# Kernel optimization log

Measured on AMD Instinct MI355X. Metric: run time of the kernel, lower is better.

The kernel has to match this reference:

```python
import jax, jax.numpy as jnp
import numpy as np

# Fixed DAG: chain 0 -> 1 -> ... -> 7 -> leaf. One activation per node.
NUM_NODES = 8          # intermediate nodes (node 7's only child is the leaf)
NUM_EDGES = NUM_NODES - 1
ACTS = ['tanh', 'relu', 'tanh', 'sigmoid', 'identity', 'relu', 'tanh', 'identity']
MAX_NORM = 25.0

_ACT_FNS = {
    'relu': jax.nn.relu,
    'tanh': jnp.tanh,
    'sigmoid': jax.nn.sigmoid,
    'identity': lambda x: x,
}


def setup_inputs() -> dict:
    key = jax.random.key(0)
    ks = jax.random.split(key, 10)
    T, B, ninp, nhid = 128, 512, 256, 256
    r = 0.1  # init_weights(0.1) uniform range
    u = lambda k, shape: jax.random.uniform(k, shape, jnp.float32, -r, r)
    return {
        'inputs': jax.random.normal(ks[0], (T, B, ninp), jnp.float32),
        'hidden': jax.random.normal(ks[1], (B, nhid), jnp.float32),
        'w_xc_w': u(ks[2], (nhid, ninp)),
        'w_xc_b': u(ks[3], (nhid,)),
        'w_xh_w': u(ks[4], (nhid, ninp)),
        'w_xh_b': u(ks[5], (nhid,)),
        'w_hc': u(ks[6], (nhid, nhid)),
        'w_hh': u(ks[7], (nhid, nhid)),
        'Wc': u(ks[8], (NUM_EDGES, nhid, nhid)),  # per-edge c-gate weights (no bias)
        'Wh': u(ks[9], (NUM_EDGES, nhid, nhid)),  # per-edge h weights (no bias)
    }


def _cell(x_t, h_prev, w_xc_w, w_xc_b, w_xh_w, w_xh_b, w_hc, w_hh, Wc, Wh):
    # node 0 (torch Linear convention: x @ W.T + b)
    c0 = jax.nn.sigmoid(x_t @ w_xc_w.T + w_xc_b + h_prev @ w_hc.T)
    f0 = _ACT_FNS[ACTS[0]]
    h = c0 * f0(x_t @ w_xh_w.T + w_xh_b + h_prev @ w_hh.T) + (1.0 - c0) * h_prev
    # chain of nodes 1..NUM_NODES-1 (fixed, small loop -> unrolled under jit)
    for e in range(NUM_EDGES):
        c = jax.nn.sigmoid(h @ Wc[e].T)
        f = _ACT_FNS[ACTS[e + 1]]
        h = c * f(h @ Wh[e].T) + (1.0 - c) * h
    # single leaf node -> mean over leaves is identity
    return h


def reference(inputs, hidden, w_xc_w, w_xc_b, w_xh_w, w_xh_b, w_hc, w_hh, Wc, Wh):
    def step(h_prev, x_t):
        out = _cell(x_t, h_prev, w_xc_w, w_xc_b, w_xh_w, w_xh_b, w_hc, w_hh, Wc, Wh)
        # NORM hidden-mode clipping: rescale rows with norm > MAX_NORM (mask is
        # computed from .data in torch, i.e. no gradient through the scale)
        norms = jnp.linalg.norm(out, axis=-1)
        scale = jax.lax.stop_gradient(jnp.where(norms > MAX_NORM, MAX_NORM / norms, 1.0))
        out = out * scale[:, None]
        return out, out  # (new hidden, per-step output) -- output == hidden here

    hidden_final, outs = jax.lax.scan(step, hidden, inputs)
    T, B, nhid = outs.shape
    outputs = outs.reshape(T * B, nhid)  # torch.cat along dim 0
    return outputs, hidden_final
```

## Files before the change

kernel.cpp:

```cpp
#include <hip/hip_runtime.h>
#include <stdint.h>


#define T_STEPS 128
#define B_ROWS  512
#define NH      256
#define NPAIRS  9
#define KQ      64

__device__ __forceinline__ float sigmoidf_(float x){
  float e = __expf(-fabsf(x));
  float s = 1.f/(1.f+e);
  return x>=0.f ? s : 1.f-s;
}
__device__ __forceinline__ float tanhf_(float x){
  float e = __expf(-2.f*fabsf(x));
  float r = (1.f-e)/(1.f+e);
  return x>=0.f ? r : -r;
}
__device__ __forceinline__ unsigned short f2bf(float f){
  uint32_t u = __float_as_uint(f);
  uint32_t r = (u + 0x7fffu + ((u>>16)&1u)) >> 16;
  return (unsigned short)r;
}
__device__ __forceinline__ uint32_t packbf(float a, float b){
  return (uint32_t)f2bf(a) | ((uint32_t)f2bf(b) << 16);
}
__device__ __forceinline__ float bfhi(float f){
  return __uint_as_float((uint32_t)f2bf(f) << 16);
}
__device__ __forceinline__ float dot2bf(uint32_t a, uint32_t b, float c){
  float d;
  asm("v_dot2_f32_bf16 %0, %1, %2, %3" : "=v"(d) : "v"(a), "v"(b), "v"(c));
  return d;
}

__global__ void prep_weights(const float* __restrict__ wxc, const float* __restrict__ wxh,
                             const float* __restrict__ whc, const float* __restrict__ whh,
                             const float* __restrict__ Wc,  const float* __restrict__ Wh,
                             uint32_t* __restrict__ WQ){
  int idx = blockIdx.x*256 + threadIdx.x;
  if (idx >= NPAIRS*KQ*NH*4) return;
  int p   = idx >> 16;
  int rem = idx & 65535;
  int kq  = rem >> 10;
  int n   = (rem >> 2) & 255;
  int c   = rem & 3;
  int mat = c & 1;
  int k0  = 4*kq + 2*(c>>1);
  const float *A, *B;
  if (p == 0)      { A = wxc; B = wxh; }
  else if (p == 1) { A = whc; B = whh; }
  else             { A = Wc + (size_t)(p-2)*NH*NH; B = Wh + (size_t)(p-2)*NH*NH; }
  const float* M = mat ? B : A;
  WQ[idx] = packbf(M[(size_t)n*NH + k0], M[(size_t)n*NH + k0 + 1]);
}

__device__ __forceinline__ void stream_q(const uint4* __restrict__ wj,
                                         const uint4* __restrict__ src,
                                         float& accA, float& accB){
  float a0=0.f,b0=0.f,a1=0.f,b1=0.f,a2=0.f,b2=0.f,a3=0.f,b3=0.f;
  #pragma unroll 8
  for (int kq = 0; kq < KQ; ++kq){
    uint4 w  = wj[(size_t)kq*NH];
    uint4 hv = src[kq];
    a0 = dot2bf(w.x, hv.x, a0);  b0 = dot2bf(w.y, hv.x, b0);
    a1 = dot2bf(w.z, hv.y, a1);  b1 = dot2bf(w.w, hv.y, b1);
    a2 = dot2bf(w.x, hv.z, a2);  b2 = dot2bf(w.y, hv.z, b2);
    a3 = dot2bf(w.z, hv.w, a3);  b3 = dot2bf(w.w, hv.w, b3);
  }
  accA += (a0 + a1) + (a2 + a3);
  accB += (b0 + b1) + (b2 + b3);
}

template<int ACT>
__device__ __forceinline__ float edge_hn(const uint4* __restrict__ wj,
                                         const uint4* __restrict__ src, float hold){
  float accA = 0.f, accB = 0.f;
  stream_q(wj, src, accA, accB);
  float c = sigmoidf_(accA);
  float f;
  if constexpr (ACT==0)      f = fmaxf(accB, 0.f);
  else if constexpr (ACT==1) f = tanhf_(accB);
  else if constexpr (ACT==2) f = sigmoidf_(accB);
  else                       f = accB;
  return c*f + (1.f-c)*hold;
}

__global__ __launch_bounds__(512) void dag_main(
    const float* __restrict__ x,
    const float* __restrict__ h0,
    const float* __restrict__ bxc,
    const float* __restrict__ bxh,
    const uint32_t* __restrict__ WQ,
    float* __restrict__ out)
{
  __shared__ float hf[2][NH];
  __shared__ uint4 hq[2][KQ];
  __shared__ uint4 xq[2][KQ];
  __shared__ float red[8];

  const int tid = threadIdx.x;
  const int j   = tid & 255;
  const int r   = tid >> 8;
  const int wv  = tid >> 6;
  const int r0  = blockIdx.x * 2;
  const uint4* WQ4 = (const uint4*)WQ;

  const int prr = tid >> 8;
  const int pc  = tid & 3;
  const int pk0 = ((tid >> 2) & 63)*4 + 2*(pc & 1);

  const float bc = bxc[j], bh = bxh[j];

  hf[r][j] = h0[(size_t)(r0 + r)*NH + j];
  __syncthreads();
  {
    float2 hp = *(const float2*)&hf[prr][pk0];
    uint32_t d = (pc < 2) ? packbf(hp.x, hp.y)
                          : packbf(hp.x - bfhi(hp.x), hp.y - bfhi(hp.y));
    ((uint32_t*)hq)[tid] = d;
    const float2 xv = *(const float2*)&x[(size_t)(r0 + prr)*NH + pk0];
    uint32_t dx = (pc < 2) ? packbf(xv.x, xv.y)
                           : packbf(xv.x - bfhi(xv.x), xv.y - bfhi(xv.y));
    ((uint32_t*)xq)[tid] = dx;
  }
  __syncthreads();

  for (int t = 0; t < T_STEPS; ++t){
    {
      float accA = 0.f, accB = 0.f;
      stream_q(WQ4 + (size_t)0*KQ*NH + j, xq[r], accA, accB);
      stream_q(WQ4 + (size_t)1*KQ*NH + j, hq[r], accA, accB);
      float hold = hf[r][j];
      float c0 = sigmoidf_(accA + bc);
      float f0 = tanhf_(accB + bh);
      hf[r][j] = c0*f0 + (1.f-c0)*hold;
    }
    __syncthreads();
    {
      float2 hp = *(const float2*)&hf[prr][pk0];
      ((uint32_t*)hq)[tid] = (pc < 2) ? packbf(hp.x, hp.y)
                                      : packbf(hp.x - bfhi(hp.x), hp.y - bfhi(hp.y));
    }
    __syncthreads();

    #define EDGE_STAGE(P, ACT)                                                   \
    hf[r][j] = edge_hn<ACT>(WQ4 + (size_t)(P)*KQ*NH + j, hq[r], hf[r][j]);       \
    __syncthreads();                                                             \
    {                                                                            \
      float2 hp = *(const float2*)&hf[prr][pk0];                                 \
      ((uint32_t*)hq)[tid] = (pc < 2) ? packbf(hp.x, hp.y)                       \
                                      : packbf(hp.x - bfhi(hp.x), hp.y - bfhi(hp.y)); \
    }                                                                            \
    __syncthreads();

    EDGE_STAGE(2, 0)
    EDGE_STAGE(3, 1)
    EDGE_STAGE(4, 2)
    EDGE_STAGE(5, 3)
    EDGE_STAGE(6, 0)
    EDGE_STAGE(7, 1)
    #undef EDGE_STAGE

    {
      float hn = edge_hn<3>(WQ4 + (size_t)8*KQ*NH + j, hq[r], hf[r][j]);
      float pw = hn*hn;
      #pragma unroll
      for (int off = 32; off; off >>= 1) pw += __shfl_xor(pw, off);
      if ((tid & 63) == 0) red[wv] = pw;
      __syncthreads();
      float s2  = red[r*4] + red[r*4+1] + red[r*4+2] + red[r*4+3];
      float nrm = sqrtf(s2);
      float sc  = (nrm > 25.f) ? 25.f/nrm : 1.f;
      float hv  = hn * sc;
      out[(size_t)t*(B_ROWS*NH) + (size_t)(r0+r)*NH + j] = hv;
      hf[r][j] = hv;
    }
    __syncthreads();
    {
      float2 hp = *(const float2*)&hf[prr][pk0];
      ((uint32_t*)hq)[tid] = (pc < 2) ? packbf(hp.x, hp.y)
                                      : packbf(hp.x - bfhi(hp.x), hp.y - bfhi(hp.y));
      if (t + 1 < T_STEPS){
        const float2 xv = *(const float2*)&x[((size_t)(t+1)*B_ROWS + r0 + prr)*NH + pk0];
        ((uint32_t*)xq)[tid] = (pc < 2) ? packbf(xv.x, xv.y)
                                        : packbf(xv.x - bfhi(xv.x), xv.y - bfhi(xv.y));
      }
    }
    __syncthreads();
  }

  out[(size_t)T_STEPS*(B_ROWS*NH) + (size_t)(r0+r)*NH + j] = hf[r][j];
}

extern "C" void kernel_launch(void* const* d_in, const int* in_sizes, int n_in,
                              void* d_out, int out_size, void* d_ws, size_t ws_size,
                              hipStream_t stream) {
  const float* x   = (const float*)d_in[0];
  const float* h0  = (const float*)d_in[1];
  const float* wxc = (const float*)d_in[2];
  const float* bxc = (const float*)d_in[3];
  const float* wxh = (const float*)d_in[4];
  const float* bxh = (const float*)d_in[5];
  const float* whc = (const float*)d_in[6];
  const float* whh = (const float*)d_in[7];
  const float* Wc  = (const float*)d_in[8];
  const float* Wh  = (const float*)d_in[9];
  uint32_t* WQ = (uint32_t*)d_ws;

  const int total = NPAIRS*KQ*NH*4;
  prep_weights<<<(total + 255)/256, 256, 0, stream>>>(wxc, wxh, whc, whh, Wc, Wh, WQ);
  dag_main<<<B_ROWS/2, 512, 0, stream>>>(x, h0, bxc, bxh, WQ, (float*)d_out);
}
```

Measured before the change: 4.788 ms.

## Switch to fp16 dot2, process four rows per block with split-K across waves

Replaces the bf16 hi/lo split representation with a single fp16 pack and v_dot2_f32_f16, halving the dot products per weight. Each 1024-thread block now handles four batch rows, with the K dimension split into four slices whose partial sums are reduced through shared memory, so every weight load is reused across four rows. Packing of h now uses wave shuffles instead of shared-memory reads. This costs some precision from fp16 rounding and adds a reduction step per stage, plus only a quarter of threads run the activations.

```diff
diff --git a/kernel.cpp b/kernel.cpp
--- a/kernel.cpp
+++ b/kernel.cpp
@@ -1,4 +1,5 @@
 #include <hip/hip_runtime.h>
+#include <hip/hip_fp16.h>
 #include <stdint.h>
 
 
@@ -7,6 +8,11 @@
 #define NH      256
 #define NPAIRS  9
 #define KQ      64
+#define BM      4
+#define NBLK    (B_ROWS/BM)
+#define NTHR    1024
+#define SQ      4
+#define QPS     (KQ/SQ)
 
 __device__ __forceinline__ float sigmoidf_(float x){
   float e = __expf(-fabsf(x));
@@ -18,20 +24,15 @@
   float r = (1.f-e)/(1.f+e);
   return x>=0.f ? r : -r;
 }
-__device__ __forceinline__ unsigned short f2bf(float f){
-  uint32_t u = __float_as_uint(f);
-  uint32_t r = (u + 0x7fffu + ((u>>16)&1u)) >> 16;
-  return (unsigned short)r;
-}
-__device__ __forceinline__ uint32_t packbf(float a, float b){
-  return (uint32_t)f2bf(a) | ((uint32_t)f2bf(b) << 16);
-}
-__device__ __forceinline__ float bfhi(float f){
-  return __uint_as_float((uint32_t)f2bf(f) << 16);
-}
-__device__ __forceinline__ float dot2bf(uint32_t a, uint32_t b, float c){
+__device__ __forceinline__ unsigned short f2h(float f){
+  return __half_as_ushort(__float2half(f));
+}
+__device__ __forceinline__ uint32_t packh(float a, float b){
+  return (uint32_t)f2h(a) | ((uint32_t)f2h(b) << 16);
+}
+__device__ __forceinline__ float fdot2_(uint32_t a, uint32_t b, float c){
   float d;
-  asm("v_dot2_f32_bf16 %0, %1, %2, %3" : "=v"(d) : "v"(a), "v"(b), "v"(c));
+  asm("v_dot2_f32_f16 %0, %1, %2, %3" : "=v"(d) : "v"(a), "v"(b), "v"(c));
   return d;
 }
 
@@ -53,41 +54,59 @@
   else if (p == 1) { A = whc; B = whh; }
   else             { A = Wc + (size_t)(p-2)*NH*NH; B = Wh + (size_t)(p-2)*NH*NH; }
   const float* M = mat ? B : A;
-  WQ[idx] = packbf(M[(size_t)n*NH + k0], M[(size_t)n*NH + k0 + 1]);
-}
-
-__device__ __forceinline__ void stream_q(const uint4* __restrict__ wj,
-                                         const uint4* __restrict__ src,
-                                         float& accA, float& accB){
-  float a0=0.f,b0=0.f,a1=0.f,b1=0.f,a2=0.f,b2=0.f,a3=0.f,b3=0.f;
-  #pragma unroll 8
-  for (int kq = 0; kq < KQ; ++kq){
-    uint4 w  = wj[(size_t)kq*NH];
-    uint4 hv = src[kq];
-    a0 = dot2bf(w.x, hv.x, a0);  b0 = dot2bf(w.y, hv.x, b0);
-    a1 = dot2bf(w.z, hv.y, a1);  b1 = dot2bf(w.w, hv.y, b1);
-    a2 = dot2bf(w.x, hv.z, a2);  b2 = dot2bf(w.y, hv.z, b2);
-    a3 = dot2bf(w.z, hv.w, a3);  b3 = dot2bf(w.w, hv.w, b3);
-  }
-  accA += (a0 + a1) + (a2 + a3);
-  accB += (b0 + b1) + (b2 + b3);
+  WQ[idx] = packh(M[(size_t)n*NH + k0], M[(size_t)n*NH + k0 + 1]);
 }
 
 template<int ACT>
-__device__ __forceinline__ float edge_hn(const uint4* __restrict__ wj,
-                                         const uint4* __restrict__ src, float hold){
-  float accA = 0.f, accB = 0.f;
-  stream_q(wj, src, accA, accB);
-  float c = sigmoidf_(accA);
-  float f;
-  if constexpr (ACT==0)      f = fmaxf(accB, 0.f);
-  else if constexpr (ACT==1) f = tanhf_(accB);
-  else if constexpr (ACT==2) f = sigmoidf_(accB);
-  else                       f = accB;
-  return c*f + (1.f-c)*hold;
-}
-
-__global__ __launch_bounds__(512) void dag_main(
+__device__ __forceinline__ float actf(float v){
+  if constexpr (ACT==0)      return fmaxf(v, 0.f);
+  else if constexpr (ACT==1) return tanhf_(v);
+  else if constexpr (ACT==2) return sigmoidf_(v);
+  else                       return v;
+}
+
+__device__ __forceinline__ void stream16(const uint4* __restrict__ wp,
+                                         const uint4 (* __restrict__ src)[2],
+                                         int qb, float* acc){
+  #pragma unroll 4
+  for (int q = 0; q < QPS; ++q){
+    const uint4 w  = wp[(size_t)q*NH];
+    const uint4 ha = src[qb+q][0];
+    const uint4 hb = src[qb+q][1];
+    acc[0]  = fdot2_(w.x, ha.x, acc[0]);
+    acc[1]  = fdot2_(w.z, ha.y, acc[1]);
+    acc[2]  = fdot2_(w.y, ha.x, acc[2]);
+    acc[3]  = fdot2_(w.w, ha.y, acc[3]);
+    acc[4]  = fdot2_(w.x, ha.z, acc[4]);
+    acc[5]  = fdot2_(w.z, ha.w, acc[5]);
+    acc[6]  = fdot2_(w.y, ha.z, acc[6]);
+    acc[7]  = fdot2_(w.w, ha.w, acc[7]);
+    acc[8]  = fdot2_(w.x, hb.x, acc[8]);
+    acc[9]  = fdot2_(w.z, hb.y, acc[9]);
+    acc[10] = fdot2_(w.y, hb.x, acc[10]);
+    acc[11] = fdot2_(w.w, hb.y, acc[11]);
+    acc[12] = fdot2_(w.x, hb.z, acc[12]);
+    acc[13] = fdot2_(w.z, hb.w, acc[13]);
+    acc[14] = fdot2_(w.y, hb.z, acc[14]);
+    acc[15] = fdot2_(w.w, hb.w, acc[15]);
+  }
+}
+
+__device__ __forceinline__ void pack_hq(uint4 (*hq)[2], int j, const float* hn){
+  uint4 v0, v1;
+  float b1, b2, b3;
+  b1=__shfl_down(hn[0],1); b2=__shfl_down(hn[0],2); b3=__shfl_down(hn[0],3);
+  v0.x = packh(hn[0], b1); v0.y = packh(b2, b3);
+  b1=__shfl_down(hn[1],1); b2=__shfl_down(hn[1],2); b3=__shfl_down(hn[1],3);
+  v0.z = packh(hn[1], b1); v0.w = packh(b2, b3);
+  b1=__shfl_down(hn[2],1); b2=__shfl_down(hn[2],2); b3=__shfl_down(hn[2],3);
+  v1.x = packh(hn[2], b1); v1.y = packh(b2, b3);
+  b1=__shfl_down(hn[3],1); b2=__shfl_down(hn[3],2); b3=__shfl_down(hn[3],3);
+  v1.z = packh(hn[3], b1); v1.w = packh(b2, b3);
+  if ((j & 3) == 0){ hq[j>>2][0] = v0; hq[j>>2][1] = v1; }
+}
+
+__global__ __launch_bounds__(NTHR) void dag_main(
     const float* __restrict__ x,
     const float* __restrict__ h0,
     const float* __restrict__ bxc,
@@ -95,65 +114,94 @@
     const uint32_t* __restrict__ WQ,
     float* __restrict__ out)
 {
-  __shared__ float hf[2][NH];
-  __shared__ uint4 hq[2][KQ];
-  __shared__ uint4 xq[2][KQ];
-  __shared__ float red[8];
+  __shared__ uint4  hq[KQ][2];
+  __shared__ uint4  xq[KQ][2];
+  __shared__ float4 part[SQ][NH][2];
+  __shared__ float  red[4][BM];
 
   const int tid = threadIdx.x;
   const int j   = tid & 255;
-  const int r   = tid >> 8;
-  const int wv  = tid >> 6;
-  const int r0  = blockIdx.x * 2;
-  const uint4* WQ4 = (const uint4*)WQ;
-
-  const int prr = tid >> 8;
-  const int pc  = tid & 3;
-  const int pk0 = ((tid >> 2) & 63)*4 + 2*(pc & 1);
-
-  const float bc = bxc[j], bh = bxh[j];
-
-  hf[r][j] = h0[(size_t)(r0 + r)*NH + j];
+  const int s   = tid >> 8;
+  const int qb  = s * QPS;
+  const int r0  = blockIdx.x * BM;
+  const uint4* WQ4   = (const uint4*)WQ;
+  const uint4* wbase = WQ4 + (size_t)qb*NH + j;
+
+  float hold[BM] = {0.f,0.f,0.f,0.f};
+  float bc = 0.f, bh = 0.f;
+  if (tid < 256){
+    bc = bxc[j]; bh = bxh[j];
+    #pragma unroll
+    for (int r = 0; r < BM; ++r) hold[r] = h0[(size_t)(r0+r)*NH + j];
+    pack_hq(hq, j, hold);
+  }
+  if (s == 3){
+    #pragma unroll
+    for (int i = 0; i < 2; ++i){
+      int d  = j + i*256;
+      int rr = d >> 7, kp = d & 127;
+      const float2 xv = *(const float2*)&x[(size_t)(r0+rr)*NH + 2*kp];
+      int kq = kp>>1, hh = rr>>1, comp = ((rr&1)<<1) | (kp&1);
+      ((uint32_t*)xq)[kq*8 + hh*4 + comp] = packh(xv.x, xv.y);
+    }
+  }
   __syncthreads();
-  {
-    float2 hp = *(const float2*)&hf[prr][pk0];
-    uint32_t d = (pc < 2) ? packbf(hp.x, hp.y)
-                          : packbf(hp.x - bfhi(hp.x), hp.y - bfhi(hp.y));
-    ((uint32_t*)hq)[tid] = d;
-    const float2 xv = *(const float2*)&x[(size_t)(r0 + prr)*NH + pk0];
-    uint32_t dx = (pc < 2) ? packbf(xv.x, xv.y)
-                           : packbf(xv.x - bfhi(xv.x), xv.y - bfhi(xv.y));
-    ((uint32_t*)xq)[tid] = dx;
-  }
-  __syncthreads();
+
+  #define STORE_PART(acc) \
+    part[s][j][0] = make_float4(acc[0]+acc[1],  acc[4]+acc[5],  acc[8]+acc[9],   acc[12]+acc[13]); \
+    part[s][j][1] = make_float4(acc[2]+acc[3],  acc[6]+acc[7],  acc[10]+acc[11], acc[14]+acc[15]);
+
+  #define SUM_PART(Av, Bv) \
+    float Av[4] = {0,0,0,0}, Bv[4] = {0,0,0,0}; \
+    _Pragma("unroll") \
+    for (int ss = 0; ss < SQ; ++ss){ \
+      float4 pa = part[ss][j][0], pb = part[ss][j][1]; \
+      Av[0]+=pa.x; Av[1]+=pa.y; Av[2]+=pa.z; Av[3]+=pa.w; \
+      Bv[0]+=pb.x; Bv[1]+=pb.y; Bv[2]+=pb.z; Bv[3]+=pb.w; \
+    }
 
   for (int t = 0; t < T_STEPS; ++t){
     {
-      float accA = 0.f, accB = 0.f;
-      stream_q(WQ4 + (size_t)0*KQ*NH + j, xq[r], accA, accB);
-      stream_q(WQ4 + (size_t)1*KQ*NH + j, hq[r], accA, accB);
-      float hold = hf[r][j];
-      float c0 = sigmoidf_(accA + bc);
-      float f0 = tanhf_(accB + bh);
-      hf[r][j] = c0*f0 + (1.f-c0)*hold;
-    }
-    __syncthreads();
-    {
-      float2 hp = *(const float2*)&hf[prr][pk0];
-      ((uint32_t*)hq)[tid] = (pc < 2) ? packbf(hp.x, hp.y)
-                                      : packbf(hp.x - bfhi(hp.x), hp.y - bfhi(hp.y));
-    }
-    __syncthreads();
-
-    #define EDGE_STAGE(P, ACT)                                                   \
-    hf[r][j] = edge_hn<ACT>(WQ4 + (size_t)(P)*KQ*NH + j, hq[r], hf[r][j]);       \
-    __syncthreads();                                                             \
-    {                                                                            \
-      float2 hp = *(const float2*)&hf[prr][pk0];                                 \
-      ((uint32_t*)hq)[tid] = (pc < 2) ? packbf(hp.x, hp.y)                       \
-                                      : packbf(hp.x - bfhi(hp.x), hp.y - bfhi(hp.y)); \
-    }                                                                            \
-    __syncthreads();
+      float acc[16] = {};
+      stream16(wbase,                    xq, qb, acc);
+      stream16(wbase + (size_t)1*KQ*NH,  hq, qb, acc);
+      STORE_PART(acc)
+      __syncthreads();
+      if (tid < 256){
+        SUM_PART(Av, Bv)
+        float hn[BM];
+        #pragma unroll
+        for (int r = 0; r < BM; ++r){
+          float c = sigmoidf_(Av[r] + bc);
+          float f = tanhf_(Bv[r] + bh);
+          hn[r] = c*f + (1.f-c)*hold[r];
+          hold[r] = hn[r];
+        }
+        pack_hq(hq, j, hn);
+      }
+      __syncthreads();
+    }
+
+    #define EDGE_STAGE(P, ACT_)                                   \
+    {                                                             \
+      float acc[16] = {};                                         \
+      stream16(wbase + (size_t)(P)*KQ*NH, hq, qb, acc);           \
+      STORE_PART(acc)                                             \
+      __syncthreads();                                            \
+      if (tid < 256){                                             \
+        SUM_PART(Av, Bv)                                          \
+        float hn[BM];                                             \
+        _Pragma("unroll")                                         \
+        for (int r = 0; r < BM; ++r){                             \
+          float c = sigmoidf_(Av[r]);                             \
+          float f = actf<ACT_>(Bv[r]);                            \
+          hn[r] = c*f + (1.f-c)*hold[r];                          \
+          hold[r] = hn[r];                                        \
+        }                                                         \
+        pack_hq(hq, j, hn);                                       \
+      }                                                           \
+      __syncthreads();                                            \
+    }
 
     EDGE_STAGE(2, 0)
     EDGE_STAGE(3, 1)
@@ -164,34 +212,60 @@
     #undef EDGE_STAGE
 
     {
-      float hn = edge_hn<3>(WQ4 + (size_t)8*KQ*NH + j, hq[r], hf[r][j]);
-      float pw = hn*hn;
-      #pragma unroll
-      for (int off = 32; off; off >>= 1) pw += __shfl_xor(pw, off);
-      if ((tid & 63) == 0) red[wv] = pw;
-      __syncthreads();
-      float s2  = red[r*4] + red[r*4+1] + red[r*4+2] + red[r*4+3];
-      float nrm = sqrtf(s2);
-      float sc  = (nrm > 25.f) ? 25.f/nrm : 1.f;
-      float hv  = hn * sc;
-      out[(size_t)t*(B_ROWS*NH) + (size_t)(r0+r)*NH + j] = hv;
-      hf[r][j] = hv;
-    }
-    __syncthreads();
-    {
-      float2 hp = *(const float2*)&hf[prr][pk0];
-      ((uint32_t*)hq)[tid] = (pc < 2) ? packbf(hp.x, hp.y)
-                                      : packbf(hp.x - bfhi(hp.x), hp.y - bfhi(hp.y));
-      if (t + 1 < T_STEPS){
-        const float2 xv = *(const float2*)&x[((size_t)(t+1)*B_ROWS + r0 + prr)*NH + pk0];
-        ((uint32_t*)xq)[tid] = (pc < 2) ? packbf(xv.x, xv.y)
-                                        : packbf(xv.x - bfhi(xv.x), xv.y - bfhi(xv.y));
-      }
-    }
-    __syncthreads();
-  }
-
-  out[(size_t)T_STEPS*(B_ROWS*NH) + (size_t)(r0+r)*NH + j] = hf[r][j];
+      float acc[16] = {};
+      stream16(wbase + (size_t)8*KQ*NH, hq, qb, acc);
+      STORE_PART(acc)
+      __syncthreads();
+      float hn[BM];
+      if (tid < 256){
+        SUM_PART(Av, Bv)
+        #pragma unroll
+        for (int r = 0; r < BM; ++r){
+          float c = sigmoidf_(Av[r]);
+          hn[r] = c*Bv[r] + (1.f-c)*hold[r];
+        }
+        #pragma unroll
+        for (int r = 0; r < BM; ++r){
+          float pw = hn[r]*hn[r];
+          #pragma unroll
+          for (int off = 32; off; off >>= 1) pw += __shfl_xor(pw, off);
+          if ((j & 63) == 0) red[j>>6][r] = pw;
+        }
+      }
+      if (s == 3 && t + 1 < T_STEPS){
+        #pragma unroll
+        for (int i = 0; i < 2; ++i){
+          int d  = j + i*256;
+          int rr = d >> 7, kp = d & 127;
+          const float2 xv = *(const float2*)&x[((size_t)(t+1)*B_ROWS + r0+rr)*NH + 2*kp];
+          int kq = kp>>1, hh = rr>>1, comp = ((rr&1)<<1) | (kp&1);
+          ((uint32_t*)xq)[kq*8 + hh*4 + comp] = packh(xv.x, xv.y);
+        }
+      }
+      __syncthreads();
+      if (tid < 256){
+        #pragma unroll
+        for (int r = 0; r < BM; ++r){
+          float n2  = red[0][r] + red[1][r] + red[2][r] + red[3][r];
+          float nrm = sqrtf(n2);
+          float sc  = (nrm > 25.f) ? 25.f/nrm : 1.f;
+          hn[r] *= sc;
+          hold[r] = hn[r];
+          out[(size_t)t*(B_ROWS*NH) + (size_t)(r0+r)*NH + j] = hn[r];
+        }
+        pack_hq(hq, j, hn);
+      }
+      __syncthreads();
+    }
+  }
+
+  if (tid < 256){
+    #pragma unroll
+    for (int r = 0; r < BM; ++r)
+      out[(size_t)T_STEPS*(B_ROWS*NH) + (size_t)(r0+r)*NH + j] = hold[r];
+  }
+  #undef STORE_PART
+  #undef SUM_PART
 }
 
 extern "C" void kernel_launch(void* const* d_in, const int* in_sizes, int n_in,
@@ -211,5 +285,5 @@
 
   const int total = NPAIRS*KQ*NH*4;
   prep_weights<<<(total + 255)/256, 256, 0, stream>>>(wxc, wxh, whc, whh, Wc, Wh, WQ);
-  dag_main<<<B_ROWS/2, 512, 0, stream>>>(x, h0, bxc, bxh, WQ, (float*)d_out);
-}
+  dag_main<<<NBLK, NTHR, 0, stream>>>(x, h0, bxc, bxh, WQ, (float*)d_out);
+}
```

After: 3.938 ms. -17.7%, faster.
